# Kernel tuning notes

Measured on AMD Instinct MI355X. Metric: run time of the kernel, lower is better.

Reference implementation:

```python
import jax, jax.numpy as jnp
import numpy as np

INPUT_DIM, HIDDEN, OUT_DIM = 7, 64, 4


def _lstm_layer(x_seq, W_ih, W_hh, b_ih, b_hh):
    """Single LSTM layer, batch_first x_seq [B,T,D] -> [B,T,H]. PyTorch gate order i,f,g,o."""
    B = x_seq.shape[0]
    H = W_hh.shape[1]
    # Precompute input projection for all timesteps (hoist GEMM out of the scan).
    x_proj = jnp.einsum('btd,gd->btg', x_seq, W_ih) + b_ih + b_hh  # [B,T,4H]

    def step(carry, xt):
        h, c = carry
        gates = xt + h @ W_hh.T  # [B,4H]
        i, f, g, o = jnp.split(gates, 4, axis=-1)
        i = jax.nn.sigmoid(i)
        f = jax.nn.sigmoid(f)
        g = jnp.tanh(g)
        o = jax.nn.sigmoid(o)
        c = f * c + i * g
        h = o * jnp.tanh(c)
        return (h, c), h

    h0 = jnp.zeros((B, H), x_seq.dtype)
    c0 = jnp.zeros((B, H), x_seq.dtype)
    (_, _), hs = jax.lax.scan(step, (h0, c0), jnp.swapaxes(x_proj, 0, 1))  # hs [T,B,H]
    return jnp.swapaxes(hs, 0, 1)  # [B,T,H]


def setup_inputs() -> dict:
    key = jax.random.key(0)
    ks = jax.random.split(key, 12)
    s = 0.1  # init scale ~ 1/sqrt(hidden)
    x = jax.random.normal(ks[0], (4096, 512, INPUT_DIM), dtype=jnp.float32)
    W_ih0 = jax.random.normal(ks[1], (4 * HIDDEN, INPUT_DIM), dtype=jnp.float32) * s
    W_hh0 = jax.random.normal(ks[2], (4 * HIDDEN, HIDDEN), dtype=jnp.float32) * s
    b_ih0 = jax.random.normal(ks[3], (4 * HIDDEN,), dtype=jnp.float32) * s
    b_hh0 = jax.random.normal(ks[4], (4 * HIDDEN,), dtype=jnp.float32) * s
    W_ih1 = jax.random.normal(ks[5], (4 * HIDDEN, HIDDEN), dtype=jnp.float32) * s
    W_hh1 = jax.random.normal(ks[6], (4 * HIDDEN, HIDDEN), dtype=jnp.float32) * s
    b_ih1 = jax.random.normal(ks[7], (4 * HIDDEN,), dtype=jnp.float32) * s
    b_hh1 = jax.random.normal(ks[8], (4 * HIDDEN,), dtype=jnp.float32) * s
    W_fc = jax.random.normal(ks[9], (OUT_DIM, HIDDEN), dtype=jnp.float32) * s
    b_fc = jax.random.normal(ks[10], (OUT_DIM,), dtype=jnp.float32) * s
    return {"x": x, "W_ih0": W_ih0, "W_hh0": W_hh0, "b_ih0": b_ih0, "b_hh0": b_hh0,
            "W_ih1": W_ih1, "W_hh1": W_hh1, "b_ih1": b_ih1, "b_hh1": b_hh1,
            "W_fc": W_fc, "b_fc": b_fc}


def reference(x, W_ih0, W_hh0, b_ih0, b_hh0, W_ih1, W_hh1, b_ih1, b_hh1, W_fc, b_fc):
    h1 = _lstm_layer(x, W_ih0, W_hh0, b_ih0, b_hh0)   # [B,T,H]
    h2 = _lstm_layer(h1, W_ih1, W_hh1, b_ih1, b_hh1)  # [B,T,H]
    last = h2[:, -1, :]                               # [B,H]
    return last @ W_fc.T + b_fc                       # [B,4]
```

## Files before the change

### kernel.cpp

```cpp
#include <hip/hip_runtime.h>

#define T_SEQ 512
#define HID 64
#define MB 16
#define NTHREADS 1024
#define A1STR 104
#define A2STR 104

typedef __attribute__((ext_vector_type(8))) short short8;
typedef __attribute__((ext_vector_type(4))) float floatx4;

#define LOG2E 1.4426950408889634f

__device__ __forceinline__ short f2bf_rne(float v) {
  unsigned u = __float_as_uint(v);
  return (short)((u + 0x7FFFu + ((u >> 16) & 1u)) >> 16);
}
__device__ __forceinline__ float rcp_(float x) { return __builtin_amdgcn_rcpf(x); }
__device__ __forceinline__ float exp2_(float x) { return __builtin_amdgcn_exp2f(x); }

__device__ __forceinline__ float gate_h(const floatx4 p, float& c) {
  float A = exp2_(-p[0]);
  float F = exp2_(-p[1]);
  float G = exp2_(p[2]);
  float O = exp2_(-p[3]);
  float ig = (G - 1.f) * rcp_((1.f + A) * (G + 1.f));
  c = rcp_(1.f + F) * c + ig;
  float C = exp2_((2.f * LOG2E) * c);
  return (C - 1.f) * rcp_((1.f + O) * (C + 1.f));
}

__device__ __forceinline__ int uofp(int p) {
  return (p & ~7) + ((p & 7) >> 1) + ((p & 1) << 2);
}

__device__ __forceinline__ short w1elem(int k, int n, float wsc,
                                        const float* __restrict__ Wih0,
                                        const float* __restrict__ Whh0) {
  float v;
  if      (k < 64) { v = Whh0[n*64 + uofp(k)]; }
  else if (k < 71) { v = Wih0[n*7 + (k - 64)]; }
  else return (short)0;
  return f2bf_rne(v * wsc);
}
__device__ __forceinline__ short w2elem(int k, int n, float wsc,
                                        const float* __restrict__ Wih1,
                                        const float* __restrict__ Whh1) {
  float v;
  if (k < 64) { v = Wih1[n*64 + uofp(k)]; }
  else        { v = Whh1[n*64 + uofp(k - 64)]; }
  return f2bf_rne(v * wsc);
}

#define MFMA(A, B, C) __builtin_amdgcn_mfma_f32_16x16x32_bf16((A), (B), (C), 0, 0, 0)

#define PACK2(ha, hb)                                                        \
  ((unsigned)(unsigned short)f2bf_rne(ha) |                                  \
   ((unsigned)(unsigned short)f2bf_rne(hb) << 16))

__global__ __launch_bounds__(NTHREADS, 4) void lstm_fused(
    const float* __restrict__ x,
    const float* __restrict__ Wih0, const float* __restrict__ Whh0,
    const float* __restrict__ bih0, const float* __restrict__ bhh0,
    const float* __restrict__ Wih1, const float* __restrict__ Whh1,
    const float* __restrict__ bih1, const float* __restrict__ bhh1,
    const float* __restrict__ Wfc,  const float* __restrict__ bfc,
    float* __restrict__ out)
{
  __shared__ __align__(16) short A1[2][MB][A1STR];
  __shared__ __align__(16) short A2[2][MB][A2STR];
  __shared__ float h2f[MB][HID + 4];

  const int tid  = threadIdx.x;
  const int lane = tid & 63;
  const int wave = tid >> 6;
  const int wl   = wave & 7;
  const bool isL1 = wave < 8;
  const int l15  = lane & 15;
  const int quad = lane >> 4;
  const int quad8= quad * 8;
  const int g4   = l15 & 3;
  const int b0   = blockIdx.x * MB;
  const int u0   = wl*8 + quad;
  const int u1   = u0 + 4;
  const int hpos = wl*8 + 2*quad;
  const int n0   = g4*64 + (wl*8 + (l15 >> 2));
  const int n1   = n0 + 4;
  const float wsc = (g4 == 2) ? 2.f * LOG2E : LOG2E;

  for (int i = tid; i < 2*MB*A1STR/2; i += NTHREADS) ((unsigned*)A1)[i] = 0u;
  for (int i = tid; i < 2*MB*A2STR/2; i += NTHREADS) ((unsigned*)A2)[i] = 0u;

  const float* bi_ = isL1 ? bih0 : bih1;
  const float* bh_ = isL1 ? bhh0 : bhh1;
  floatx4 bia, bib;
  #pragma unroll
  for (int g = 0; g < 4; ++g) {
    float ws = (g == 2) ? 2.f * LOG2E : LOG2E;
    bia[g] = (bi_[g*64 + u0] + bh_[g*64 + u0]) * ws;
    bib[g] = (bi_[g*64 + u1] + bh_[g*64 + u1]) * ws;
  }

  const int xd   = lane & 31;
  const int xrow = 2*wl + (lane >> 5);
  const bool xact = isL1 && (xd < 7);
  const float* xbase = x + ((size_t)(b0 + xrow) * T_SEQ) * 7 + xd;
  float xcur = 0.f;
  if (xact) {
    A1[0][xrow][64 + xd] = f2bf_rne(xbase[0]);
    xcur = xbase[7];
  }

  short8 WA[4], WB[4];
  if (isL1) {
    #pragma unroll
    for (int ks = 0; ks < 3; ++ks) {
      short8 fa, fb;
      #pragma unroll
      for (int jj = 0; jj < 8; ++jj) {
        fa[jj] = w1elem(ks*32 + quad8 + jj, n0, wsc, Wih0, Whh0);
        fb[jj] = w1elem(ks*32 + quad8 + jj, n1, wsc, Wih0, Whh0);
      }
      WA[ks] = fa; WB[ks] = fb;
    }
  } else {
    #pragma unroll
    for (int ks = 0; ks < 4; ++ks) {
      short8 fa, fb;
      #pragma unroll
      for (int jj = 0; jj < 8; ++jj) {
        fa[jj] = w2elem(ks*32 + quad8 + jj, n0, wsc, Wih1, Whh1);
        fb[jj] = w2elem(ks*32 + quad8 + jj, n1, wsc, Wih1, Whh1);
      }
      WA[ks] = fa; WB[ks] = fb;
    }
  }
  __syncthreads();

  float ca = 0.f, cb = 0.f;

#define STEP_X(NXT, XT)                                                      \
    if (xact) {                                                              \
      A1[NXT][xrow][64 + xd] = f2bf_rne(xcur);                               \
      xcur = xbase[7 * (XT)];                                                \
    }

#define STEP_FULL(CUR, NXT, IT)                                              \
  {                                                                          \
    if (isL1) {                                                              \
      int xt_ = (IT) + 2; if (xt_ > T_SEQ - 1) xt_ = T_SEQ - 1;              \
      STEP_X(NXT, xt_)                                                       \
      short8 hf0 = *(const short8*)&A1[CUR][l15][     quad8];                \
      short8 hf1 = *(const short8*)&A1[CUR][l15][32 + quad8];                \
      short8 hfx = *(const short8*)&A1[CUR][l15][64 + quad8];                \
      floatx4 pa = bia, pb = bib;                                            \
      pa = MFMA(WA[0], hf0, pa);  pb = MFMA(WB[0], hf0, pb);                 \
      pa = MFMA(WA[1], hf1, pa);  pb = MFMA(WB[1], hf1, pb);                 \
      pa = MFMA(WA[2], hfx, pa);  pb = MFMA(WB[2], hfx, pb);                 \
      float ha = gate_h(pa, ca);                                             \
      float hb = gate_h(pb, cb);                                             \
      *(unsigned*)&A1[NXT][l15][hpos] = PACK2(ha, hb);                       \
    } else {                                                                 \
      short8 hf0 = *(const short8*)&A1[CUR][l15][     quad8];                \
      short8 hf1 = *(const short8*)&A1[CUR][l15][32 + quad8];                \
      short8 h20 = *(const short8*)&A2[CUR][l15][     quad8];                \
      short8 h21 = *(const short8*)&A2[CUR][l15][32 + quad8];                \
      floatx4 pa = bia, pb = bib;                                            \
      pa = MFMA(WA[0], hf0, pa);  pb = MFMA(WB[0], hf0, pb);                 \
      pa = MFMA(WA[1], hf1, pa);  pb = MFMA(WB[1], hf1, pb);                 \
      pa = MFMA(WA[2], h20, pa);  pb = MFMA(WB[2], h20, pb);                 \
      pa = MFMA(WA[3], h21, pa);  pb = MFMA(WB[3], h21, pb);                 \
      float ha = gate_h(pa, ca);                                             \
      float hb = gate_h(pb, cb);                                             \
      *(unsigned*)&A2[NXT][l15][hpos] = PACK2(ha, hb);                       \
    }                                                                        \
    __syncthreads();                                                         \
  }

  {
    if (isL1) {
      STEP_X(1, 2)
      short8 hf0 = *(const short8*)&A1[0][l15][     quad8];
      short8 hf1 = *(const short8*)&A1[0][l15][32 + quad8];
      short8 hfx = *(const short8*)&A1[0][l15][64 + quad8];
      floatx4 pa = bia, pb = bib;
      pa = MFMA(WA[0], hf0, pa);  pb = MFMA(WB[0], hf0, pb);
      pa = MFMA(WA[1], hf1, pa);  pb = MFMA(WB[1], hf1, pb);
      pa = MFMA(WA[2], hfx, pa);  pb = MFMA(WB[2], hfx, pb);
      float ha = gate_h(pa, ca);
      float hb = gate_h(pb, cb);
      *(unsigned*)&A1[1][l15][hpos] = PACK2(ha, hb);
    }
    __syncthreads();
  }

  #pragma unroll 1
  for (int k = 0; k < 255; ++k) {
    STEP_FULL(1, 0, 2*k + 1)
    STEP_FULL(0, 1, 2*k + 2)
  }
  STEP_FULL(1, 0, 511)

  {
    if (!isL1) {
      short8 hf0 = *(const short8*)&A1[0][l15][     quad8];
      short8 hf1 = *(const short8*)&A1[0][l15][32 + quad8];
      short8 h20 = *(const short8*)&A2[0][l15][     quad8];
      short8 h21 = *(const short8*)&A2[0][l15][32 + quad8];
      floatx4 pa = bia, pb = bib;
      pa = MFMA(WA[0], hf0, pa);  pb = MFMA(WB[0], hf0, pb);
      pa = MFMA(WA[1], hf1, pa);  pb = MFMA(WB[1], hf1, pb);
      pa = MFMA(WA[2], h20, pa);  pb = MFMA(WB[2], h20, pb);
      pa = MFMA(WA[3], h21, pa);  pb = MFMA(WB[3], h21, pb);
      h2f[l15][u0] = gate_h(pa, ca);
      h2f[l15][u1] = gate_h(pb, cb);
    }
    __syncthreads();
  }

  if (tid < MB * 4) {
    int bbf = tid >> 2, o = tid & 3;
    float acc = bfc[o];
    #pragma unroll 8
    for (int kk = 0; kk < HID; ++kk) acc += h2f[bbf][kk] * Wfc[o*HID + kk];
    out[(size_t)(b0 + bbf) * 4 + o] = acc;
  }
}

extern "C" void kernel_launch(void* const* d_in, const int* in_sizes, int n_in,
                              void* d_out, int out_size, void* d_ws, size_t ws_size,
                              hipStream_t stream) {
  const float* x    = (const float*)d_in[0];
  const float* Wih0 = (const float*)d_in[1];
  const float* Whh0 = (const float*)d_in[2];
  const float* bih0 = (const float*)d_in[3];
  const float* bhh0 = (const float*)d_in[4];
  const float* Wih1 = (const float*)d_in[5];
  const float* Whh1 = (const float*)d_in[6];
  const float* bih1 = (const float*)d_in[7];
  const float* bhh1 = (const float*)d_in[8];
  const float* Wfc  = (const float*)d_in[9];
  const float* bfc  = (const float*)d_in[10];
  (void)d_ws; (void)ws_size; (void)n_in; (void)out_size;

  const int B = in_sizes[0] / (T_SEQ * 7);
  dim3 grid(B / MB);
  lstm_fused<<<grid, NTHREADS, 0, stream>>>(x, Wih0, Whh0, bih0, bhh0,
                                            Wih1, Whh1, bih1, bhh1, Wfc, bfc,
                                            (float*)d_out);
}
```

Before: 436.1 us.

## Feed x fragments straight from global into registers and trim the per-step gate math

Layer-1 input x is now loaded per row directly from global memory into registers. It is converted to a bf16 MFMA operand with the hardware v_cvt_pk_bf16_f32 instruction, one step ahead, instead of being staged through the shared-memory A1 buffer. The gate update is rewritten to merge two reciprocals into one, and the hidden-state pack also uses the packed convert. MFMA blocks are wrapped in s_setprio to favour the matrix issue. This shortens the per-timestep critical path of the latency-bound recurrence, at the cost of redundant global loads across quads and slightly different rounding in the cell update.

Result: no change. 443.0 us (+1.6%).

```diff
diff --git a/kernel.cpp b/kernel.cpp
--- a/kernel.cpp
+++ b/kernel.cpp
@@ -9,6 +9,7 @@
 
 typedef __attribute__((ext_vector_type(8))) short short8;
 typedef __attribute__((ext_vector_type(4))) float floatx4;
+typedef float floatx4u __attribute__((ext_vector_type(4), aligned(4)));
 
 #define LOG2E 1.4426950408889634f
 
@@ -18,16 +19,33 @@
 }
 __device__ __forceinline__ float rcp_(float x) { return __builtin_amdgcn_rcpf(x); }
 __device__ __forceinline__ float exp2_(float x) { return __builtin_amdgcn_exp2f(x); }
+
+__device__ __forceinline__ unsigned cvt_pk_bf16(float lo, float hi) {
+  unsigned r;
+  asm("v_cvt_pk_bf16_f32 %0, %1, %2" : "=v"(r) : "v"(lo), "v"(hi));
+  return r;
+}
 
 __device__ __forceinline__ float gate_h(const floatx4 p, float& c) {
   float A = exp2_(-p[0]);
   float F = exp2_(-p[1]);
   float G = exp2_(p[2]);
   float O = exp2_(-p[3]);
-  float ig = (G - 1.f) * rcp_((1.f + A) * (G + 1.f));
-  c = rcp_(1.f + F) * c + ig;
+  float t1 = (1.f + A) * (G + 1.f);
+  float t2 = 1.f + F;
+  float num = c * t1 + (G - 1.f) * t2;
+  c = num * rcp_(t1 * t2);
   float C = exp2_((2.f * LOG2E) * c);
   return (C - 1.f) * rcp_((1.f + O) * (C + 1.f));
+}
+
+__device__ __forceinline__ short8 xcvt(floatx4 lo, float x4, float x5, float x6) {
+  union { unsigned u[4]; short8 s; } r;
+  r.u[0] = cvt_pk_bf16(lo[0], lo[1]);
+  r.u[1] = cvt_pk_bf16(lo[2], lo[3]);
+  r.u[2] = cvt_pk_bf16(x4, x5);
+  r.u[3] = cvt_pk_bf16(x6, 0.f);
+  return r.s;
 }
 
 __device__ __forceinline__ int uofp(int p) {
@@ -53,10 +71,6 @@
 }
 
 #define MFMA(A, B, C) __builtin_amdgcn_mfma_f32_16x16x32_bf16((A), (B), (C), 0, 0, 0)
-
-#define PACK2(ha, hb)                                                        \
-  ((unsigned)(unsigned short)f2bf_rne(ha) |                                  \
-   ((unsigned)(unsigned short)f2bf_rne(hb) << 16))
 
 __global__ __launch_bounds__(NTHREADS, 4) void lstm_fused(
     const float* __restrict__ x,
@@ -101,14 +115,11 @@
     bib[g] = (bi_[g*64 + u1] + bh_[g*64 + u1]) * ws;
   }
 
-  const int xd   = lane & 31;
-  const int xrow = 2*wl + (lane >> 5);
-  const bool xact = isL1 && (xd < 7);
-  const float* xbase = x + ((size_t)(b0 + xrow) * T_SEQ) * 7 + xd;
-  float xcur = 0.f;
-  if (xact) {
-    A1[0][xrow][64 + xd] = f2bf_rne(xbase[0]);
-    xcur = xbase[7];
+  const float* xrow = x + (size_t)(b0 + l15) * (T_SEQ * 7);
+  short8 xfrag = {};
+  if (isL1) {
+    floatx4 lo = *(const floatx4u*)xrow;
+    xfrag = xcvt(lo, xrow[4], xrow[5], xrow[6]);
   }
 
   short8 WA[4], WB[4];
@@ -139,57 +150,59 @@
 
   float ca = 0.f, cb = 0.f;
 
-#define STEP_X(NXT, XT)                                                      \
-    if (xact) {                                                              \
-      A1[NXT][xrow][64 + xd] = f2bf_rne(xcur);                               \
-      xcur = xbase[7 * (XT)];                                                \
-    }
-
 #define STEP_FULL(CUR, NXT, IT)                                              \
   {                                                                          \
     if (isL1) {                                                              \
-      int xt_ = (IT) + 2; if (xt_ > T_SEQ - 1) xt_ = T_SEQ - 1;              \
-      STEP_X(NXT, xt_)                                                       \
+      int xt_ = (IT) + 1; if (xt_ > T_SEQ - 1) xt_ = T_SEQ - 1;              \
+      const float* xp_ = xrow + 7 * xt_;                                     \
+      floatx4 nlo = *(const floatx4u*)xp_;                                   \
+      float nx4 = xp_[4], nx5 = xp_[5], nx6 = xp_[6];                        \
       short8 hf0 = *(const short8*)&A1[CUR][l15][     quad8];                \
       short8 hf1 = *(const short8*)&A1[CUR][l15][32 + quad8];                \
-      short8 hfx = *(const short8*)&A1[CUR][l15][64 + quad8];                \
       floatx4 pa = bia, pb = bib;                                            \
+      __builtin_amdgcn_s_setprio(1);                                         \
       pa = MFMA(WA[0], hf0, pa);  pb = MFMA(WB[0], hf0, pb);                 \
       pa = MFMA(WA[1], hf1, pa);  pb = MFMA(WB[1], hf1, pb);                 \
-      pa = MFMA(WA[2], hfx, pa);  pb = MFMA(WB[2], hfx, pb);                 \
+      pa = MFMA(WA[2], xfrag, pa); pb = MFMA(WB[2], xfrag, pb);              \
+      __builtin_amdgcn_s_setprio(0);                                         \
       float ha = gate_h(pa, ca);                                             \
       float hb = gate_h(pb, cb);                                             \
-      *(unsigned*)&A1[NXT][l15][hpos] = PACK2(ha, hb);                       \
+      *(unsigned*)&A1[NXT][l15][hpos] = cvt_pk_bf16(ha, hb);                 \
+      xfrag = xcvt(nlo, nx4, nx5, nx6);                                      \
     } else {                                                                 \
       short8 hf0 = *(const short8*)&A1[CUR][l15][     quad8];                \
       short8 hf1 = *(const short8*)&A1[CUR][l15][32 + quad8];                \
       short8 h20 = *(const short8*)&A2[CUR][l15][     quad8];                \
       short8 h21 = *(const short8*)&A2[CUR][l15][32 + quad8];                \
       floatx4 pa = bia, pb = bib;                                            \
+      __builtin_amdgcn_s_setprio(1);                                         \
       pa = MFMA(WA[0], hf0, pa);  pb = MFMA(WB[0], hf0, pb);                 \
       pa = MFMA(WA[1], hf1, pa);  pb = MFMA(WB[1], hf1, pb);                 \
       pa = MFMA(WA[2], h20, pa);  pb = MFMA(WB[2], h20, pb);                 \
       pa = MFMA(WA[3], h21, pa);  pb = MFMA(WB[3], h21, pb);                 \
+      __builtin_amdgcn_s_setprio(0);                                         \
       float ha = gate_h(pa, ca);                                             \
       float hb = gate_h(pb, cb);                                             \
-      *(unsigned*)&A2[NXT][l15][hpos] = PACK2(ha, hb);                       \
+      *(unsigned*)&A2[NXT][l15][hpos] = cvt_pk_bf16(ha, hb);                 \
     }                                                                        \
     __syncthreads();                                                         \
   }
 
   {
     if (isL1) {
-      STEP_X(1, 2)
+      const float* xp_ = xrow + 7;
+      floatx4 nlo = *(const floatx4u*)xp_;
+      float nx4 = xp_[4], nx5 = xp_[5], nx6 = xp_[6];
       short8 hf0 = *(const short8*)&A1[0][l15][     quad8];
       short8 hf1 = *(const short8*)&A1[0][l15][32 + quad8];
-      short8 hfx = *(const short8*)&A1[0][l15][64 + quad8];
       floatx4 pa = bia, pb = bib;
       pa = MFMA(WA[0], hf0, pa);  pb = MFMA(WB[0], hf0, pb);
       pa = MFMA(WA[1], hf1, pa);  pb = MFMA(WB[1], hf1, pb);
-      pa = MFMA(WA[2], hfx, pa);  pb = MFMA(WB[2], hfx, pb);
+      pa = MFMA(WA[2], xfrag, pa); pb = MFMA(WB[2], xfrag, pb);
       float ha = gate_h(pa, ca);
       float hb = gate_h(pb, cb);
-      *(unsigned*)&A1[1][l15][hpos] = PACK2(ha, hb);
+      *(unsigned*)&A1[1][l15][hpos] = cvt_pk_bf16(ha, hb);
+      xfrag = xcvt(nlo, nx4, nx5, nx6);
     }
     __syncthreads();
   }
```
